# Performance work log

Hardware: AMD Instinct MI355X
Metric: run time of the kernel (lower is better)

## Reference

```python
import jax, jax.numpy as jnp
import numpy as np

NB_HEAD = 8
SIZE_PER_HEAD = 64
MAX_LEN = 1024
MASK_PENALTY = 1e12


def setup_inputs() -> dict:
    key = jax.random.key(0)
    ks = jax.random.split(key, 6)
    B, L, D_IN = 8, MAX_LEN, 512
    D_OUT = NB_HEAD * SIZE_PER_HEAD
    return {
        "Q_seq": jax.random.normal(ks[0], (B, L, D_IN), dtype=jnp.float32),
        "K_seq": jax.random.normal(ks[1], (B, L, D_IN), dtype=jnp.float32),
        "V_seq": jax.random.normal(ks[2], (B, L, D_IN), dtype=jnp.float32),
        "WQ": jax.random.normal(ks[3], (D_IN, D_OUT), dtype=jnp.float32) * 0.03,
        "WK": jax.random.normal(ks[4], (D_IN, D_OUT), dtype=jnp.float32) * 0.03,
        "WV": jax.random.normal(ks[5], (D_IN, D_OUT), dtype=jnp.float32) * 0.03,
    }


def reference(Q_seq, K_seq, V_seq, WQ, WK, WV):
    B, L, _ = Q_seq.shape
    H, D = NB_HEAD, SIZE_PER_HEAD
    # project and split heads: [B, L, H*D] -> [B, H, L, D]
    q = (Q_seq @ WQ).reshape(B, L, H, D).transpose(0, 2, 1, 3)
    k = (K_seq @ WK).reshape(B, L, H, D).transpose(0, 2, 1, 3)
    v = (V_seq @ WV).reshape(B, L, H, D).transpose(0, 2, 1, 3)
    scale = 1.0 / jnp.sqrt(jnp.asarray(D, dtype=q.dtype))
    scores = jnp.einsum('bhqd,bhkd->bhqk', q, k) * scale  # [B,H,L,L]
    # Mask(): eye+cumsum construction == causal mask (penalize key > query)
    causal = jnp.triu(jnp.ones((L, L), dtype=scores.dtype), k=1)
    scores = scores - causal * MASK_PENALTY
    A = jax.nn.softmax(scores, axis=-1)
    O = jnp.einsum('bhqk,bhkd->bhqd', A, v)  # [B,H,L,D]
    return O.transpose(0, 2, 1, 3).reshape(B, L, H * D)
```

## Files before the change

kernel.cpp:

```cpp
#include <hip/hip_runtime.h>

#define NH 8
#define DH 64
#define SL 1024
#define NB 8
#define DIN 512
#define DOUT 512
#define PS 72

typedef __bf16 bf16x8 __attribute__((ext_vector_type(8)));
typedef float floatx4 __attribute__((ext_vector_type(4)));
typedef unsigned short ushortx4 __attribute__((ext_vector_type(4)));
typedef unsigned short ushortx8 __attribute__((ext_vector_type(8)));

__device__ __forceinline__ unsigned short f2bf(float f) {
    unsigned int u = __builtin_bit_cast(unsigned int, f);
    u += 0x7FFFu + ((u >> 16) & 1u);
    return (unsigned short)(u >> 16);
}

__device__ __forceinline__ floatx4 mfma_bf16(bf16x8 a, bf16x8 b, floatx4 c) {
    return __builtin_amdgcn_mfma_f32_16x16x32_bf16(a, b, c, 0, 0, 0);
}

__device__ __forceinline__ void gld_lds16(const unsigned short* g, unsigned short* l) {
    __builtin_amdgcn_global_load_lds(
        (const __attribute__((address_space(1))) unsigned int*)g,
        (__attribute__((address_space(3))) unsigned int*)l, 16, 0, 0);
}

__global__ __launch_bounds__(256) void xbf_kernel(const float* __restrict__ Qs,
                                                  const float* __restrict__ Ks,
                                                  const float* __restrict__ Vs,
                                                  unsigned short* __restrict__ xb) {
    const int z = blockIdx.y;
    const float* X = (z == 0) ? Qs : (z == 1 ? Ks : Vs);
    const int t = blockIdx.x * 256 + threadIdx.x;
    const int row = t >> 6, c = t & 63;
    const float4 a = *(const float4*)(X + t * 8);
    const float4 b = *(const float4*)(X + t * 8 + 4);
    ushortx8 o;
    o[0] = f2bf(a.x); o[1] = f2bf(a.y); o[2] = f2bf(a.z); o[3] = f2bf(a.w);
    o[4] = f2bf(b.x); o[5] = f2bf(b.y); o[6] = f2bf(b.z); o[7] = f2bf(b.w);
    const int dst = (((row >> 7) * 8 + (c >> 3)) * 128 + (row & 127)) * 64 +
                    (((c & 7) ^ (row & 7)) * 8);
    *(ushortx8*)(xb + z * 8192 * DIN + dst) = o;
}

__global__ __launch_bounds__(256) void wt_kernel(const float* __restrict__ WQ,
                                                 const float* __restrict__ WK,
                                                 const float* __restrict__ WV,
                                                 unsigned short* __restrict__ wt) {
    __shared__ unsigned short tile[64][68];
    const int z = blockIdx.z;
    const float* W = (z == 0) ? WQ : (z == 1 ? WK : WV);
    const int k0 = blockIdx.y * 64, n0 = blockIdx.x * 64;
    const int tn = threadIdx.x & 63, tk = threadIdx.x >> 6;
#pragma unroll
    for (int i = 0; i < 16; ++i) {
        const int kk = tk + i * 4;
        tile[tn][kk] = f2bf(W[(k0 + kk) * DOUT + n0 + tn]);
    }
    __syncthreads();
#pragma unroll
    for (int i = 0; i < 16; ++i) {
        const int nn = tk + i * 4;
        const int n = n0 + nn, k = k0 + tn;
        const int dst = (((z * 4 + (n >> 7)) * 8 + (k >> 6)) * 128 + (n & 127)) * 64 +
                        ((((k >> 3) & 7) ^ (n & 7)) * 8) + (k & 7);
        wt[dst] = tile[nn][tn];
    }
}

__global__ __launch_bounds__(256) void proj_kernel(const unsigned short* __restrict__ xbt,
                                                   const unsigned short* __restrict__ wtt,
                                                   unsigned short* __restrict__ qw,
                                                   unsigned short* __restrict__ ks,
                                                   unsigned short* __restrict__ vs) {
    __shared__ __align__(16) unsigned short As[128 * 64];
    __shared__ __align__(16) unsigned short Bs[128 * 64];
    const int z = blockIdx.z;
    const int mblk = blockIdx.x, nblk = blockIdx.y;
    const int w = threadIdx.x >> 6, lane = threadIdx.x & 63;
    const int l15 = lane & 15, quad = lane >> 4;
    const int wm = w >> 1, wn = w & 1;
    const int soff = lane * 8;
    const unsigned short* Ab = xbt + z * (8192 * DIN) + mblk * 8 * 8192 + (w * 4) * 512 + soff;
    const unsigned short* Bb = wtt + (z * 4 + nblk) * 8 * 8192 + (w * 4) * 512 + soff;
    unsigned short* Asw = &As[(w * 4) * 512];
    unsigned short* Bsw = &Bs[(w * 4) * 512];

    floatx4 acc[4][4];
#pragma unroll
    for (int i = 0; i < 4; ++i)
#pragma unroll
        for (int j = 0; j < 4; ++j) acc[i][j] = floatx4{0.f, 0.f, 0.f, 0.f};

    for (int kblk = 0; kblk < 8; ++kblk) {
        __syncthreads();
#pragma unroll
        for (int i = 0; i < 4; ++i) {
            gld_lds16(Ab + kblk * 8192 + i * 512, Asw + i * 512);
            gld_lds16(Bb + kblk * 8192 + i * 512, Bsw + i * 512);
        }
        __syncthreads();
#pragma unroll
        for (int ksub = 0; ksub < 2; ++ksub) {
            bf16x8 af[4], bfr[4];
#pragma unroll
            for (int mi = 0; mi < 4; ++mi) {
                const int row = wm * 64 + mi * 16 + l15;
                af[mi] = *(const bf16x8*)&As[row * 64 + (((quad + ksub * 4) ^ (l15 & 7)) * 8)];
            }
#pragma unroll
            for (int nt = 0; nt < 4; ++nt) {
                const int row = wn * 64 + nt * 16 + l15;
                bfr[nt] = *(const bf16x8*)&Bs[row * 64 + (((quad + ksub * 4) ^ (l15 & 7)) * 8)];
            }
#pragma unroll
            for (int mi = 0; mi < 4; ++mi)
#pragma unroll
                for (int nt = 0; nt < 4; ++nt)
                    acc[mi][nt] = mfma_bf16(af[mi], bfr[nt], acc[mi][nt]);
        }
    }

#pragma unroll
    for (int mi = 0; mi < 4; ++mi)
#pragma unroll
        for (int nt = 0; nt < 4; ++nt)
#pragma unroll
            for (int r = 0; r < 4; ++r) {
                const int grow = mblk * 128 + wm * 64 + mi * 16 + quad * 4 + r;
                const int gcol = nblk * 128 + wn * 64 + nt * 16 + l15;
                const int b = grow >> 10, li = grow & 1023;
                const int h = gcol >> 6, d = gcol & 63;
                const int bh = b * NH + h;
                const float v = acc[mi][nt][r];
                if (z == 0) {
                    qw[(bh * SL + li) * DH + d] = f2bf(v * 0.125f);
                } else if (z == 1) {
                    const int idx = ((bh * 64 + (li >> 4)) * 2 + (d >> 5)) * 512 +
                                    (li & 15) * 32 + (d & 31);
                    ks[idx] = f2bf(v);
                } else {
                    const int s64 = ((li & 15) << 2) | ((li >> 4) & 3);
                    const int idx = ((bh * 32 + ((li >> 6) << 1) + (s64 >> 5)) * 64 + d) * 32 +
                                    (s64 & 31);
                    vs[idx] = f2bf(v);
                }
            }
}

__global__ __launch_bounds__(256) void attn_kernel(const unsigned short* __restrict__ qw,
                                                   const unsigned short* __restrict__ ksp,
                                                   const unsigned short* __restrict__ vsp,
                                                   float* __restrict__ out) {
    __shared__ unsigned short Ps[4][16 * PS];
    __shared__ float Cb[2][64][21];
    const int w = threadIdx.x >> 6;
    const int lane = threadIdx.x & 63;
    const int l15 = lane & 15, quad = lane >> 4;
    const int bh = blockIdx.y;
    const int b = bh >> 3, h = bh & 7;
    const int tile = (w < 2) ? blockIdx.x : 63 - blockIdx.x;
    const int half = w & 1;
    const int m0 = tile * 16;

    const unsigned short* qp = qw + (bh * SL + m0 + l15) * DH + quad * 8;
    const bf16x8 aQ0 = *(const bf16x8*)qp;
    const bf16x8 aQ1 = *(const bf16x8*)(qp + 32);

    const unsigned short* ksb = ksp + (bh * 64) * 2 * 512 + l15 * 32 + quad * 8;
    const unsigned short* vsb = vsp + (bh * 32 * 64 + l15) * 32 + quad * 8;
    unsigned short* myPs = Ps[w];

    float lrow[4] = {0.f, 0.f, 0.f, 0.f};
    floatx4 o0 = {0.f, 0.f, 0.f, 0.f}, o1 = o0, o2 = o0, o3 = o0;
    const floatx4 zf = {0.f, 0.f, 0.f, 0.f};

    auto LK = [&](int kt, bf16x8* kf) {
        const unsigned short* kp = ksb + (kt >> 4) * 1024;
#pragma unroll
        for (int t = 0; t < 4; ++t) {
            kf[t * 2]     = *(const bf16x8*)(kp + t * 1024);
            kf[t * 2 + 1] = *(const bf16x8*)(kp + t * 1024 + 512);
        }
    };

    auto TAIL = [&](int kt, floatx4* s, bool domask, const bf16x8* v0, const bf16x8* v1) {
#pragma unroll
        for (int r = 0; r < 4; ++r) {
            const int row = m0 + quad * 4 + r;
            float p[4];
#pragma unroll
            for (int t = 0; t < 4; ++t) {
                float e = __expf(s[t][r]);
                if (domask && (kt + t * 16 + l15 > row)) e = 0.f;
                p[t] = e;
            }
            lrow[r] += (p[0] + p[1]) + (p[2] + p[3]);
            ushortx4 pk;
            pk[0] = f2bf(p[0]); pk[1] = f2bf(p[1]);
            pk[2] = f2bf(p[2]); pk[3] = f2bf(p[3]);
            *(ushortx4*)(myPs + (quad * 4 + r) * PS + l15 * 4) = pk;
        }
        __builtin_amdgcn_wave_barrier();
        const bf16x8 aP0 = *(const bf16x8*)(myPs + l15 * PS + quad * 8);
        const bf16x8 aP1 = *(const bf16x8*)(myPs + l15 * PS + 32 + quad * 8);
        __builtin_amdgcn_wave_barrier();
        o0 = mfma_bf16(aP1, v1[0], mfma_bf16(aP0, v0[0], o0));
        o1 = mfma_bf16(aP1, v1[1], mfma_bf16(aP0, v0[1], o1));
        o2 = mfma_bf16(aP1, v1[2], mfma_bf16(aP0, v0[2], o2));
        o3 = mfma_bf16(aP1, v1[3], mfma_bf16(aP0, v0[3], o3));
    };

    auto BODY = [&](int kt, const bf16x8* kf) {
        const unsigned short* vb = vsb + (kt >> 5) * 2048;
        bf16x8 v0[4], v1[4];
#pragma unroll
        for (int dt = 0; dt < 4; ++dt) {
            v0[dt] = *(const bf16x8*)(vb + dt * 512);
            v1[dt] = *(const bf16x8*)(vb + dt * 512 + 2048);
        }
        floatx4 s[4];
#pragma unroll
        for (int t = 0; t < 4; ++t)
            s[t] = mfma_bf16(aQ1, kf[t * 2 + 1], mfma_bf16(aQ0, kf[t * 2], zf));
        TAIL(kt, s, false, v0, v1);
    };

    auto BODYM = [&](int kt) {
        const unsigned short* vb = vsb + (kt >> 5) * 2048;
        bf16x8 v0[4], v1[4];
#pragma unroll
        for (int dt = 0; dt < 4; ++dt) {
            v0[dt] = *(const bf16x8*)(vb + dt * 512);
            v1[dt] = *(const bf16x8*)(vb + dt * 512 + 2048);
        }
        const unsigned short* kp = ksb + (kt >> 4) * 1024;
        floatx4 s[4] = {zf, zf, zf, zf};
#pragma unroll
        for (int t = 0; t < 4; ++t) {
            if (kt + t * 16 <= m0 + 15) {
                const bf16x8 k0 = *(const bf16x8*)(kp + t * 1024);
                const bf16x8 k1 = *(const bf16x8*)(kp + t * 1024 + 512);
                s[t] = mfma_bf16(aQ1, k1, mfma_bf16(aQ0, k0, zf));
            }
        }
        TAIL(kt, s, true, v0, v1);
    };

    bf16x8 ka[8], kb2[8];
    const int nf = (tile + 4) >> 2;
    const int last = nf - 1;
    int j = half;
    if (j < last) LK(j * 64, ka);
    while (j + 2 < last) {
        LK((j + 2) * 64, kb2);
        BODY(j * 64, ka);
        if (j + 4 < last) LK((j + 4) * 64, ka);
        BODY((j + 2) * 64, kb2);
        j += 4;
    }
    if (j < last) { BODY(j * 64, ka); j += 2; }
    if ((last & 1) == half) BODYM(last * 64);

    if (half == 1) {
        float* cb = &Cb[w >> 1][lane][0];
#pragma unroll
        for (int r = 0; r < 4; ++r) {
            cb[r] = o0[r]; cb[4 + r] = o1[r];
            cb[8 + r] = o2[r]; cb[12 + r] = o3[r];
            cb[16 + r] = lrow[r];
        }
    }
    __syncthreads();
    if (half == 0) {
        const float* cb = &Cb[w >> 1][lane][0];
#pragma unroll
        for (int r = 0; r < 4; ++r) {
            o0[r] += cb[r]; o1[r] += cb[4 + r];
            o2[r] += cb[8 + r]; o3[r] += cb[12 + r];
            lrow[r] += cb[16 + r];
        }
#pragma unroll
        for (int r = 0; r < 4; ++r) {
            float l = lrow[r];
            l += __shfl_xor(l, 1);
            l += __shfl_xor(l, 2);
            l += __shfl_xor(l, 4);
            l += __shfl_xor(l, 8);
            const float inv = 1.0f / l;
            const int row = m0 + quad * 4 + r;
            float* op = out + (b * SL + row) * DOUT + h * DH + l15;
            op[0]  = o0[r] * inv;
            op[16] = o1[r] * inv;
            op[32] = o2[r] * inv;
            op[48] = o3[r] * inv;
        }
    }
}

extern "C" void kernel_launch(void* const* d_in, const int* in_sizes, int n_in,
                              void* d_out, int out_size, void* d_ws, size_t ws_size,
                              hipStream_t stream) {
    const float* Qs = (const float*)d_in[0];
    const float* Ks = (const float*)d_in[1];
    const float* Vs = (const float*)d_in[2];
    const float* WQ = (const float*)d_in[3];
    const float* WK = (const float*)d_in[4];
    const float* WV = (const float*)d_in[5];
    float* out = (float*)d_out;

    unsigned short* xb = (unsigned short*)d_ws;
    unsigned short* wt = xb + 3 * 8192 * DIN;
    unsigned short* qw = wt + 3 * DIN * DOUT;
    unsigned short* ks = qw + NB * NH * SL * DH;
    unsigned short* vs = ks + NB * NH * SL * DH;

    xbf_kernel<<<dim3(8192 * DIN / (256 * 8), 3), 256, 0, stream>>>(Qs, Ks, Vs, xb);
    wt_kernel<<<dim3(DOUT / 64, DIN / 64, 3), 256, 0, stream>>>(WQ, WK, WV, wt);
    proj_kernel<<<dim3(64, 4, 3), 256, 0, stream>>>(xb, wt, qw, ks, vs);
    attn_kernel<<<dim3(32, NB * NH), 256, 0, stream>>>(qw, ks, vs, out);
}
```

Baseline: 174.9 us.

## Stage projection epilogue through LDS, use exp2, simplify attention K loads

The projection epilogue now writes results into shared memory in the destination layout and then copies them out with coalesced 16-byte stores, replacing scattered 2-byte global stores. Q is scaled by 0.125*log2(e) so the attention softmax can call the native exp2 instead of __expf. The P tile is packed to bf16 with a byte-permute (truncation rather than round-to-nearest), and the P and reduction buffers share one LDS union, which cuts LDS use and may raise occupancy. The hand-written double-buffered K prefetch is replaced by a simple loop that loads K inline, trading explicit latency hiding for lower register pressure.

After: 166.3 us. 4.9% less time.

```diff
diff --git a/kernel.cpp b/kernel.cpp
--- a/kernel.cpp
+++ b/kernel.cpp
@@ -10,7 +10,6 @@
 
 typedef __bf16 bf16x8 __attribute__((ext_vector_type(8)));
 typedef float floatx4 __attribute__((ext_vector_type(4)));
-typedef unsigned short ushortx4 __attribute__((ext_vector_type(4)));
 typedef unsigned short ushortx8 __attribute__((ext_vector_type(8)));
 
 __device__ __forceinline__ unsigned short f2bf(float f) {
@@ -27,6 +26,11 @@
     __builtin_amdgcn_global_load_lds(
         (const __attribute__((address_space(1))) unsigned int*)g,
         (__attribute__((address_space(3))) unsigned int*)l, 16, 0, 0);
+}
+
+__device__ __forceinline__ unsigned int pack_bf2(float a, float b) {
+    return __builtin_amdgcn_perm(__builtin_bit_cast(unsigned int, b),
+                                 __builtin_bit_cast(unsigned int, a), 0x07060302u);
 }
 
 __global__ __launch_bounds__(256) void xbf_kernel(const float* __restrict__ Qs,
@@ -77,8 +81,9 @@
                                                    unsigned short* __restrict__ qw,
                                                    unsigned short* __restrict__ ks,
                                                    unsigned short* __restrict__ vs) {
-    __shared__ __align__(16) unsigned short As[128 * 64];
-    __shared__ __align__(16) unsigned short Bs[128 * 64];
+    __shared__ __align__(16) unsigned short S[16384];
+    unsigned short* As = S;
+    unsigned short* Bs = S + 8192;
     const int z = blockIdx.z;
     const int mblk = blockIdx.x, nblk = blockIdx.y;
     const int w = threadIdx.x >> 6, lane = threadIdx.x & 63;
@@ -125,39 +130,66 @@
         }
     }
 
+    __syncthreads();
 #pragma unroll
     for (int mi = 0; mi < 4; ++mi)
 #pragma unroll
         for (int nt = 0; nt < 4; ++nt)
 #pragma unroll
             for (int r = 0; r < 4; ++r) {
-                const int grow = mblk * 128 + wm * 64 + mi * 16 + quad * 4 + r;
-                const int gcol = nblk * 128 + wn * 64 + nt * 16 + l15;
-                const int b = grow >> 10, li = grow & 1023;
-                const int h = gcol >> 6, d = gcol & 63;
-                const int bh = b * NH + h;
-                const float v = acc[mi][nt][r];
+                const int a = wm * 64 + mi * 16 + quad * 4 + r;
+                const int c = wn * 64 + nt * 16 + l15;
+                const int h = c >> 6, dh = c & 63;
+                float v = acc[mi][nt][r];
+                int lidx;
                 if (z == 0) {
-                    qw[(bh * SL + li) * DH + d] = f2bf(v * 0.125f);
+                    v *= 0.18033688f;
+                    lidx = h * 8192 + a * 64 + dh;
                 } else if (z == 1) {
-                    const int idx = ((bh * 64 + (li >> 4)) * 2 + (d >> 5)) * 512 +
-                                    (li & 15) * 32 + (d & 31);
-                    ks[idx] = f2bf(v);
+                    lidx = (((((h << 3) + (a >> 4)) << 1) | (dh >> 5))) * 512 +
+                           (a & 15) * 32 + (dh & 31);
                 } else {
-                    const int s64 = ((li & 15) << 2) | ((li >> 4) & 3);
-                    const int idx = ((bh * 32 + ((li >> 6) << 1) + (s64 >> 5)) * 64 + d) * 32 +
-                                    (s64 & 31);
-                    vs[idx] = f2bf(v);
+                    const int s64 = ((a & 15) << 2) | ((a >> 4) & 3);
+                    lidx = ((((h << 1) | (a >> 6)) << 1) | (s64 >> 5)) * 2048 +
+                           dh * 32 + (s64 & 31);
                 }
-            }
+                S[lidx] = f2bf(v);
+            }
+    __syncthreads();
+
+    const int b = mblk >> 3;
+    const int li0 = (mblk & 7) * 128;
+    const int tid = threadIdx.x;
+    unsigned short* outp = (z == 0) ? qw : (z == 1 ? ks : vs);
+#pragma unroll
+    for (int j = 0; j < 8; ++j) {
+        const int off = j * 2048 + tid * 8;
+        const ushortx8 val = *(const ushortx8*)(S + off);
+        int gidx;
+        if (z == 0) {
+            const int h = off >> 13, rem = off & 8191;
+            gidx = ((b * 8 + nblk * 2 + h) * 1024 + li0) * 64 + rem;
+        } else if (z == 1) {
+            const int region = off >> 9, pos = off & 511;
+            const int h = region >> 4, g = (region >> 1) & 7, d5 = region & 1;
+            gidx = (((b * 8 + nblk * 2 + h) * 64 + (li0 >> 4) + g) * 2 + d5) * 512 + pos;
+        } else {
+            const int region = off >> 11, pos = off & 2047;
+            const int h = region >> 2, l6 = (region >> 1) & 1, s5 = region & 1;
+            gidx = ((b * 8 + nblk * 2 + h) * 32 + (li0 >> 5) + l6 * 2 + s5) * 2048 + pos;
+        }
+        *(ushortx8*)(outp + gidx) = val;
+    }
 }
 
 __global__ __launch_bounds__(256) void attn_kernel(const unsigned short* __restrict__ qw,
                                                    const unsigned short* __restrict__ ksp,
                                                    const unsigned short* __restrict__ vsp,
                                                    float* __restrict__ out) {
-    __shared__ unsigned short Ps[4][16 * PS];
-    __shared__ float Cb[2][64][21];
+    __shared__ union {
+        unsigned short Ps[4][16 * PS];
+        float Cb[2][64][21];
+    } sh;
     const int w = threadIdx.x >> 6;
     const int lane = threadIdx.x & 63;
     const int l15 = lane & 15, quad = lane >> 4;
@@ -173,21 +205,12 @@
 
     const unsigned short* ksb = ksp + (bh * 64) * 2 * 512 + l15 * 32 + quad * 8;
     const unsigned short* vsb = vsp + (bh * 32 * 64 + l15) * 32 + quad * 8;
-    unsigned short* myPs = Ps[w];
+    unsigned short* myPs = sh.Ps[w];
 
     float lrow[4] = {0.f, 0.f, 0.f, 0.f};
     floatx4 o0 = {0.f, 0.f, 0.f, 0.f}, o1 = o0, o2 = o0, o3 = o0;
     const floatx4 zf = {0.f, 0.f, 0.f, 0.f};
 
-    auto LK = [&](int kt, bf16x8* kf) {
-        const unsigned short* kp = ksb + (kt >> 4) * 1024;
-#pragma unroll
-        for (int t = 0; t < 4; ++t) {
-            kf[t * 2]     = *(const bf16x8*)(kp + t * 1024);
-            kf[t * 2 + 1] = *(const bf16x8*)(kp + t * 1024 + 512);
-        }
-    };
-
     auto TAIL = [&](int kt, floatx4* s, bool domask, const bf16x8* v0, const bf16x8* v1) {
 #pragma unroll
         for (int r = 0; r < 4; ++r) {
@@ -195,15 +218,15 @@
             float p[4];
 #pragma unroll
             for (int t = 0; t < 4; ++t) {
-                float e = __expf(s[t][r]);
+                float e = __builtin_amdgcn_exp2f(s[t][r]);
                 if (domask && (kt + t * 16 + l15 > row)) e = 0.f;
                 p[t] = e;
             }
             lrow[r] += (p[0] + p[1]) + (p[2] + p[3]);
-            ushortx4 pk;
-            pk[0] = f2bf(p[0]); pk[1] = f2bf(p[1]);
-            pk[2] = f2bf(p[2]); pk[3] = f2bf(p[3]);
-            *(ushortx4*)(myPs + (quad * 4 + r) * PS + l15 * 4) = pk;
+            uint2 pk;
+            pk.x = pack_bf2(p[0], p[1]);
+            pk.y = pack_bf2(p[2], p[3]);
+            *(uint2*)(myPs + (quad * 4 + r) * PS + l15 * 4) = pk;
         }
         __builtin_amdgcn_wave_barrier();
         const bf16x8 aP0 = *(const bf16x8*)(myPs + l15 * PS + quad * 8);
@@ -215,7 +238,7 @@
         o3 = mfma_bf16(aP1, v1[3], mfma_bf16(aP0, v0[3], o3));
     };
 
-    auto BODY = [&](int kt, const bf16x8* kf) {
+    auto BODY = [&](int kt) {
         const unsigned short* vb = vsb + (kt >> 5) * 2048;
         bf16x8 v0[4], v1[4];
 #pragma unroll
@@ -223,10 +246,14 @@
             v0[dt] = *(const bf16x8*)(vb + dt * 512);
             v1[dt] = *(const bf16x8*)(vb + dt * 512 + 2048);
         }
+        const unsigned short* kp = ksb + (kt >> 4) * 1024;
         floatx4 s[4];
 #pragma unroll
-        for (int t = 0; t < 4; ++t)
-            s[t] = mfma_bf16(aQ1, kf[t * 2 + 1], mfma_bf16(aQ0, kf[t * 2], zf));
+        for (int t = 0; t < 4; ++t) {
+            const bf16x8 k0 = *(const bf16x8*)(kp + t * 1024);
+            const bf16x8 k1 = *(const bf16x8*)(kp + t * 1024 + 512);
+            s[t] = mfma_bf16(aQ1, k1, mfma_bf16(aQ0, k0, zf));
+        }
         TAIL(kt, s, false, v0, v1);
     };
 
@@ -251,23 +278,14 @@
         TAIL(kt, s, true, v0, v1);
     };
 
-    bf16x8 ka[8], kb2[8];
     const int nf = (tile + 4) >> 2;
     const int last = nf - 1;
-    int j = half;
-    if (j < last) LK(j * 64, ka);
-    while (j + 2 < last) {
-        LK((j + 2) * 64, kb2);
-        BODY(j * 64, ka);
-        if (j + 4 < last) LK((j + 4) * 64, ka);
-        BODY((j + 2) * 64, kb2);
-        j += 4;
-    }
-    if (j < last) { BODY(j * 64, ka); j += 2; }
+    for (int j = half; j < last; j += 2) BODY(j * 64);
     if ((last & 1) == half) BODYM(last * 64);
 
+    __syncthreads();
     if (half == 1) {
-        float* cb = &Cb[w >> 1][lane][0];
+        float* cb = &sh.Cb[w >> 1][lane][0];
 #pragma unroll
         for (int r = 0; r < 4; ++r) {
             cb[r] = o0[r]; cb[4 + r] = o1[r];
@@ -277,7 +295,7 @@
     }
     __syncthreads();
     if (half == 0) {
-        const float* cb = &Cb[w >> 1][lane][0];
+        const float* cb = &sh.Cb[w >> 1][lane][0];
 #pragma unroll
         for (int r = 0; r < 4; ++r) {
             o0[r] += cb[r]; o1[r] += cb[4 + r];
```
